# Performance work log

Measured on AMD Instinct MI355X. Metric: run time of the kernel, lower is better.

The kernel has to match this reference:

```python
import jax, jax.numpy as jnp
import numpy as np

GAMMA = 1.0        # softmin temperature
BANDWIDTH = 0      # 0 => no Sakoe-Chiba band (numba code only skips when 0 < bw < |i-j|)
BIG = 1e30         # finite stand-in for +inf: exp(-BIG/gamma) underflows to exactly 0 in fp32,
                   # reproducing the inf-initialized R/SigR softmin ratios without NaNs
B, N, M = 32, 512, 512


def setup_inputs() -> dict:
    k1, k2 = jax.random.split(jax.random.key(0))
    D = jax.random.uniform(k1, (B, N, M), dtype=jnp.float32)    # pairwise distances (>= 0)
    Sig = jax.random.uniform(k2, (B, N, M), dtype=jnp.float32)  # per-cell uncertainty
    return {"D": D, "Sig": Sig}


def _soft_dtw(D, Sig):
    """uDTW forward DP (compute_softdtw), vectorized over anti-diagonal wavefronts.
    Returns jnp.stack([R[:, N, M], SigR[:, N, M]]) of shape (2, B)."""
    b, n, m = D.shape
    alpha = 1.0 / GAMMA
    # Dp[i, j] == D_new[i, j] = D[i-1, j-1] with zero border (indices 0..N, 0..M)
    Dp = jnp.pad(D, ((0, 0), (1, 0), (1, 0)))
    Sp = jnp.pad(Sig, ((0, 0), (1, 0), (1, 0)))
    iarr = jnp.arange(n + 1)

    def diag(A, d):
        # A[:, i, d - i] for i = 0..N, zero where j out of [0, M]
        j = d - iarr
        vals = A[:, iarr, jnp.clip(j, 0, m)]
        return jnp.where((j >= 0) & (j <= m), vals, 0.0)

    def shift(x, fill):
        # x[:, i-1] (index i-1 along the diagonal buffer)
        return jnp.concatenate([jnp.full((b, 1), fill, x.dtype), x[:, :-1]], axis=1)

    # diagonal buffers indexed by i; diag d=0 holds R[0,0]=0, rest inf(BIG); diag d=1 all inf
    r2 = jnp.full((b, n + 1), BIG, jnp.float32).at[:, 0].set(0.0)
    r1 = jnp.full((b, n + 1), BIG, jnp.float32)
    s2 = jnp.full((b, n + 1), BIG, jnp.float32).at[:, 0].set(0.0)
    s1 = jnp.full((b, n + 1), BIG, jnp.float32)

    def step(carry, d):
        r2, r1, s2, s1 = carry  # R/SigR diagonals d-2 and d-1
        j = d - iarr
        valid = (iarr >= 1) & (j >= 1) & (j <= m)
        if BANDWIDTH > 0:
            valid = valid & (jnp.abs(iarr - j) <= BANDWIDTH)
        # softmin ratios from R neighbors: (i-1,j-1)=prev2 shifted, (i-1,j)=prev1 shifted, (i,j-1)=prev1
        rr0 = -alpha * shift(r2, BIG)
        rr1 = -alpha * shift(r1, BIG)
        rr2 = -alpha * r1
        rmax = jnp.maximum(jnp.maximum(rr0, rr1), rr2)
        e0 = jnp.exp(rr0 - rmax)
        e1 = jnp.exp(rr1 - rmax)
        e2 = jnp.exp(rr2 - rmax)
        inv = 1.0 / (e0 + e1 + e2)
        p0, p1, p2 = e0 * inv, e1 * inv, e2 * inv
        dDd, dD1, dD2 = diag(Dp, d), diag(Dp, d - 1), diag(Dp, d - 2)
        dSd, dS1, dS2 = diag(Sp, d), diag(Sp, d - 1), diag(Sp, d - 2)
        # R[i,j] = D[i-1,j-1] + softmin-weighted avg of D_new neighbors (uDTW recurrence)
        newR = jnp.where(valid, dDd + p0 * shift(dD2, 0.0) + p1 * shift(dD1, 0.0) + p2 * dD1, BIG)
        newS = jnp.where(valid, dSd + p0 * shift(dS2, 0.0) + p1 * shift(dS1, 0.0) + p2 * dS1, BIG)
        return (r1, newR, s1, newS), None

    (_, rlast, _, slast), _ = jax.lax.scan(step, (r2, r1, s2, s1), jnp.arange(2, n + m + 1))
    # last anti-diagonal d = N + M contains cell (N, M) at index i = N
    return jnp.stack([rlast[:, n], slast[:, n]])  # (2, B)


def reference(D, Sig):
    return _soft_dtw(D, Sig)
```

## Files before the change

### kernel.cpp

```cpp
#include <hip/hip_runtime.h>


constexpr int N = 512;
constexpr int M = 512;
constexpr int BATCH = 32;
constexpr int NM = N + M;
constexpr int K = 32;
constexpr int NB = 32;
constexpr int PHASES = NB + 7;
constexpr float NL2E = -1.4426950408889634f;
constexpr float NLN2 = -0.6931471805599453f;
constexpr float EPS  = 1e-30f;

__device__ __forceinline__ float lane_shr1_or(float oldv, float x) {
  return __int_as_float(__builtin_amdgcn_update_dpp(
      __float_as_int(oldv), __float_as_int(x), 0x138, 0xf, 0xf, false));
}
__device__ __forceinline__ int qclamp(int q) {
  return q < 0 ? 0 : (q > 127 ? 127 : q);
}

__global__ __launch_bounds__(512, 2)
void softdtw_fwd(const float* __restrict__ D,
                 const float* __restrict__ Sig,
                 float* __restrict__ out) {
  const int b = blockIdx.x;
  const int t = threadIdx.x;
  const int w = t >> 6;
  const float4* Drow4 = (const float4*)(D + ((size_t)b * N + t) * M);

  __shared__ float2 edge[8][640];
  __shared__ __align__(16) float zpad[64];
  for (int idx = t; idx < 8 * 640; idx += 512)
    ((float2*)edge)[idx] = make_float2(0.f, 0.f);
  if (t < 64) zpad[t] = 0.f;

  float eSelf = 0.f, dSelfL = 0.f;
  float eN2 = (t == 0) ? 1.f : 0.f, dN2L = 0.f;

  const int Bl = 2 * w, Bh = 2 * w + 17;

  float4 r0, r1, r2, r3, r4, r5, r6, r7, r8;
  {
    const int q = (32 * Bl - t) >> 2;
    r0 = Drow4[qclamp(q + 0)]; r1 = Drow4[qclamp(q + 1)];
    r2 = Drow4[qclamp(q + 2)]; r3 = Drow4[qclamp(q + 3)];
    r4 = Drow4[qclamp(q + 4)]; r5 = Drow4[qclamp(q + 5)];
    r6 = Drow4[qclamp(q + 6)]; r7 = Drow4[qclamp(q + 7)];
    r8 = Drow4[qclamp(q + 8)];
  }
  __syncthreads();

  for (int p = 0; p < PHASES; ++p) {
    const int B = p - w;
    const int nB = B + 1;
    const bool dopre = (nB >= Bl) && (nB <= Bh);

    if (B >= Bl && B <= Bh) {
      const int d0 = 2 + B * K;
      const int c0 = d0 - t - 2;

      const float4* ep = (w > 0)
          ? (const float4*)&edge[w - 1][64 + (d0 - 64 * w - 2)]
          : (const float4*)zpad;

      const float4 n0 = ep[0], n1 = ep[1], n2 = ep[2], n3 = ep[3];

      const int s = c0 & 3;
      const bool s2 = (s & 2) != 0, s1b = (s & 1) != 0;
      const float
        f0 = r0.x, f1 = r0.y, f2 = r0.z, f3 = r0.w,
        f4 = r1.x, f5 = r1.y, f6 = r1.z, f7 = r1.w,
        f8 = r2.x, f9 = r2.y, f10 = r2.z, f11 = r2.w,
        f12 = r3.x, f13 = r3.y, f14 = r3.z, f15 = r3.w,
        f16 = r4.x, f17 = r4.y, f18 = r4.z, f19 = r4.w,
        f20 = r5.x, f21 = r5.y, f22 = r5.z, f23 = r5.w,
        f24 = r6.x, f25 = r6.y, f26 = r6.z, f27 = r6.w,
        f28 = r7.x, f29 = r7.y, f30 = r7.z, f31 = r7.w,
        f32 = r8.x, f33 = r8.y, f34 = r8.z, f35 = r8.w;
      const float
        x0  = s2 ? f2  : f0,  x1  = s2 ? f3  : f1,  x2  = s2 ? f4  : f2,
        x3  = s2 ? f5  : f3,  x4  = s2 ? f6  : f4,  x5  = s2 ? f7  : f5,
        x6  = s2 ? f8  : f6,  x7  = s2 ? f9  : f7,  x8  = s2 ? f10 : f8,
        x9  = s2 ? f11 : f9,  x10 = s2 ? f12 : f10, x11 = s2 ? f13 : f11,
        x12 = s2 ? f14 : f12, x13 = s2 ? f15 : f13, x14 = s2 ? f16 : f14,
        x15 = s2 ? f17 : f15, x16 = s2 ? f18 : f16, x17 = s2 ? f19 : f17,
        x18 = s2 ? f20 : f18, x19 = s2 ? f21 : f19, x20 = s2 ? f22 : f20,
        x21 = s2 ? f23 : f21, x22 = s2 ? f24 : f22, x23 = s2 ? f25 : f23,
        x24 = s2 ? f26 : f24, x25 = s2 ? f27 : f25, x26 = s2 ? f28 : f26,
        x27 = s2 ? f29 : f27, x28 = s2 ? f30 : f28, x29 = s2 ? f31 : f29,
        x30 = s2 ? f32 : f30, x31 = s2 ? f33 : f31, x32 = s2 ? f34 : f32;
      const float
        g0  = s1b ? x1  : x0,  g1  = s1b ? x2  : x1,  g2  = s1b ? x3  : x2,
        g3  = s1b ? x4  : x3,  g4  = s1b ? x5  : x4,  g5  = s1b ? x6  : x5,
        g6  = s1b ? x7  : x6,  g7  = s1b ? x8  : x7,  g8  = s1b ? x9  : x8,
        g9  = s1b ? x10 : x9,  g10 = s1b ? x11 : x10, g11 = s1b ? x12 : x11,
        g12 = s1b ? x13 : x12, g13 = s1b ? x14 : x13, g14 = s1b ? x15 : x14,
        g15 = s1b ? x16 : x15, g16 = s1b ? x17 : x16, g17 = s1b ? x18 : x17,
        g18 = s1b ? x19 : x18, g19 = s1b ? x20 : x19, g20 = s1b ? x21 : x20,
        g21 = s1b ? x22 : x21, g22 = s1b ? x23 : x22, g23 = s1b ? x24 : x23,
        g24 = s1b ? x25 : x24, g25 = s1b ? x26 : x25, g26 = s1b ? x27 : x26,
        g27 = s1b ? x28 : x27, g28 = s1b ? x29 : x28, g29 = s1b ? x30 : x29,
        g30 = s1b ? x31 : x30, g31 = s1b ? x32 : x31;

      if (dopre) {
        const int q = (32 * nB - t) >> 2;
        r0 = Drow4[qclamp(q + 0)]; r1 = Drow4[qclamp(q + 1)];
        r2 = Drow4[qclamp(q + 2)]; r3 = Drow4[qclamp(q + 3)];
        r4 = Drow4[qclamp(q + 4)]; r5 = Drow4[qclamp(q + 5)];
        r6 = Drow4[qclamp(q + 6)]; r7 = Drow4[qclamp(q + 7)];
        r8 = Drow4[qclamp(q + 8)];
      }

      const float4 n4 = ep[4], n5 = ep[5], n6 = ep[6], n7 = ep[7];

      float2* eput = &edge[w][64 + c0];

#define STEP(kk, NE, ND)                                                       \
      {                                                                        \
        const int c = c0 + (kk);                                               \
        const bool valid = ((unsigned)c) < 512u;                               \
        const float ddL = (g##kk) * NL2E;                                      \
        const float ddLm = valid ? ddL : -1e30f;                               \
        const float sE = lane_shr1_or((NE), eSelf);                            \
        const float sD = lane_shr1_or((ND), dSelfL);                           \
        const float e0 = eN2, e2 = eSelf;                                      \
        const float s02 = (e0 + e2) + EPS;                                     \
        const float sum = s02 + sE;                                            \
        const float inv = __builtin_amdgcn_rcpf(sum);                          \
        const float numL = fmaf(e0, dN2L, fmaf(sE, sD, e2 * dSelfL));          \
        const float rr = fmaf(inv, numL, ddLm);                                \
        const float newE = __builtin_amdgcn_exp2f(rr);                         \
        if (d0 + (kk) == NM && t == N - 1) {                                   \
          const float* Sb = Sig + (size_t)b * N * M;                           \
          const float sgA = Sb[(size_t)(N - 1) * M + (M - 1)];                 \
          const float sg0 = Sb[(size_t)(N - 2) * M + (M - 2)];                 \
          const float sg1 = Sb[(size_t)(N - 2) * M + (M - 1)];                 \
          const float sg2 = Sb[(size_t)(N - 1) * M + (M - 2)];                 \
          out[b] = rr * NLN2;                                                  \
          out[BATCH + b] = sgA + inv * (e0 * sg0 + sE * sg1 + e2 * sg2);       \
        }                                                                      \
        eN2 = sE; dN2L = sD;                                                   \
        eSelf = newE; dSelfL = ddL;                                            \
        eput[kk] = make_float2(newE, ddL);                                     \
      }
#define STEP2(m, NQ)                                                           \
      STEP(2 * m,     NQ.x, NQ.y)                                              \
      STEP(2 * m + 1, NQ.z, NQ.w)

      STEP(0,  n0.x, n0.y)  STEP(1,  n0.z, n0.w)
      STEP(2,  n1.x, n1.y)  STEP(3,  n1.z, n1.w)
      STEP(4,  n2.x, n2.y)  STEP(5,  n2.z, n2.w)
      STEP(6,  n3.x, n3.y)  STEP(7,  n3.z, n3.w)

      const float4 n8 = ep[8], n9 = ep[9], n10 = ep[10], n11 = ep[11];

      STEP(8,  n4.x, n4.y)  STEP(9,  n4.z, n4.w)
      STEP(10, n5.x, n5.y)  STEP(11, n5.z, n5.w)
      STEP(12, n6.x, n6.y)  STEP(13, n6.z, n6.w)
      STEP(14, n7.x, n7.y)  STEP(15, n7.z, n7.w)

      const float4 n12 = ep[12], n13 = ep[13], n14 = ep[14], n15 = ep[15];

      STEP(16, n8.x,  n8.y)   STEP(17, n8.z,  n8.w)
      STEP(18, n9.x,  n9.y)   STEP(19, n9.z,  n9.w)
      STEP(20, n10.x, n10.y)  STEP(21, n10.z, n10.w)
      STEP(22, n11.x, n11.y)  STEP(23, n11.z, n11.w)

      STEP(24, n12.x, n12.y)  STEP(25, n12.z, n12.w)
      STEP(26, n13.x, n13.y)  STEP(27, n13.z, n13.w)
      STEP(28, n14.x, n14.y)  STEP(29, n14.z, n14.w)
      STEP(30, n15.x, n15.y)  STEP(31, n15.z, n15.w)
#undef STEP2
#undef STEP
    } else if (dopre) {
      const int q = (32 * nB - t) >> 2;
      r0 = Drow4[qclamp(q + 0)]; r1 = Drow4[qclamp(q + 1)];
      r2 = Drow4[qclamp(q + 2)]; r3 = Drow4[qclamp(q + 3)];
      r4 = Drow4[qclamp(q + 4)]; r5 = Drow4[qclamp(q + 5)];
      r6 = Drow4[qclamp(q + 6)]; r7 = Drow4[qclamp(q + 7)];
      r8 = Drow4[qclamp(q + 8)];
    }

    __syncthreads();
  }
}

extern "C" void kernel_launch(void* const* d_in, const int* in_sizes, int n_in,
                              void* d_out, int out_size, void* d_ws, size_t ws_size,
                              hipStream_t stream) {
  const float* D   = (const float*)d_in[0];
  const float* Sig = (const float*)d_in[1];
  float* out = (float*)d_out;
  softdtw_fwd<<<dim3(BATCH), dim3(512), 0, stream>>>(D, Sig, out);
}
```

Before: 177.8 us.

## Double wavefront block width to halve phase count and barriers

Raises the diagonal block size from 32 to 64, so each wave processes 64 anti-diagonal steps per phase and the number of block-synchronised phases drops from 39 to 23. It prefetches the next D block in two chunks interleaved with the compute, and replaces __syncthreads with an explicit LDS wait plus a raw s_barrier. The aim is to cut barrier and pipeline fill/drain overhead. In exchange, register pressure roughly doubles for the D window (17 float4s plus 64 selected values) at 512 threads with 2 blocks per SM, which risks spills, and the raw barrier skips the vmcnt wait.

```diff
diff --git a/kernel.cpp b/kernel.cpp
--- a/kernel.cpp
+++ b/kernel.cpp
@@ -5,9 +5,9 @@
 constexpr int M = 512;
 constexpr int BATCH = 32;
 constexpr int NM = N + M;
-constexpr int K = 32;
-constexpr int NB = 32;
-constexpr int PHASES = NB + 7;
+constexpr int K = 64;
+constexpr int NB = 16;
+constexpr int PHASES = 23;
 constexpr float NL2E = -1.4426950408889634f;
 constexpr float NLN2 = -0.6931471805599453f;
 constexpr float EPS  = 1e-30f;
@@ -30,89 +30,64 @@
   const float4* Drow4 = (const float4*)(D + ((size_t)b * N + t) * M);
 
   __shared__ float2 edge[8][640];
-  __shared__ __align__(16) float zpad[64];
+  __shared__ __align__(16) float zpad[128];
   for (int idx = t; idx < 8 * 640; idx += 512)
     ((float2*)edge)[idx] = make_float2(0.f, 0.f);
-  if (t < 64) zpad[t] = 0.f;
+  if (t < 128) zpad[t] = 0.f;
 
   float eSelf = 0.f, dSelfL = 0.f;
   float eN2 = (t == 0) ? 1.f : 0.f, dN2L = 0.f;
 
-  const int Bl = 2 * w, Bh = 2 * w + 17;
-
-  float4 r0, r1, r2, r3, r4, r5, r6, r7, r8;
+  const int Bl = w, Bh = w + 8;
+
+  float4 r0,r1,r2,r3,r4,r5,r6,r7,r8,r9,r10,r11,r12,r13,r14,r15,r16;
   {
-    const int q = (32 * Bl - t) >> 2;
-    r0 = Drow4[qclamp(q + 0)]; r1 = Drow4[qclamp(q + 1)];
-    r2 = Drow4[qclamp(q + 2)]; r3 = Drow4[qclamp(q + 3)];
-    r4 = Drow4[qclamp(q + 4)]; r5 = Drow4[qclamp(q + 5)];
-    r6 = Drow4[qclamp(q + 6)]; r7 = Drow4[qclamp(q + 7)];
-    r8 = Drow4[qclamp(q + 8)];
+    const int q = (K * Bl - t) >> 2;
+    r0 = Drow4[qclamp(q + 0)];  r1 = Drow4[qclamp(q + 1)];
+    r2 = Drow4[qclamp(q + 2)];  r3 = Drow4[qclamp(q + 3)];
+    r4 = Drow4[qclamp(q + 4)];  r5 = Drow4[qclamp(q + 5)];
+    r6 = Drow4[qclamp(q + 6)];  r7 = Drow4[qclamp(q + 7)];
+    r8 = Drow4[qclamp(q + 8)];  r9 = Drow4[qclamp(q + 9)];
+    r10 = Drow4[qclamp(q + 10)]; r11 = Drow4[qclamp(q + 11)];
+    r12 = Drow4[qclamp(q + 12)]; r13 = Drow4[qclamp(q + 13)];
+    r14 = Drow4[qclamp(q + 14)]; r15 = Drow4[qclamp(q + 15)];
+    r16 = Drow4[qclamp(q + 16)];
   }
   __syncthreads();
 
   for (int p = 0; p < PHASES; ++p) {
     const int B = p - w;
-    const int nB = B + 1;
-    const bool dopre = (nB >= Bl) && (nB <= Bh);
+    const int Bn = B + 1;
+    const bool dopre = (Bn >= Bl) && (Bn <= Bh);
 
     if (B >= Bl && B <= Bh) {
       const int d0 = 2 + B * K;
-      const int c0 = d0 - t - 2;
+      const int c0 = K * B - t;
 
       const float4* ep = (w > 0)
-          ? (const float4*)&edge[w - 1][64 + (d0 - 64 * w - 2)]
+          ? (const float4*)&edge[w - 1][64 + K * (B - w)]
           : (const float4*)zpad;
 
-      const float4 n0 = ep[0], n1 = ep[1], n2 = ep[2], n3 = ep[3];
+      const float4 na0 = ep[0], na1 = ep[1], na2 = ep[2], na3 = ep[3];
 
       const int s = c0 & 3;
       const bool s2 = (s & 2) != 0, s1b = (s & 1) != 0;
-      const float
-        f0 = r0.x, f1 = r0.y, f2 = r0.z, f3 = r0.w,
-        f4 = r1.x, f5 = r1.y, f6 = r1.z, f7 = r1.w,
-        f8 = r2.x, f9 = r2.y, f10 = r2.z, f11 = r2.w,
-        f12 = r3.x, f13 = r3.y, f14 = r3.z, f15 = r3.w,
-        f16 = r4.x, f17 = r4.y, f18 = r4.z, f19 = r4.w,
-        f20 = r5.x, f21 = r5.y, f22 = r5.z, f23 = r5.w,
-        f24 = r6.x, f25 = r6.y, f26 = r6.z, f27 = r6.w,
-        f28 = r7.x, f29 = r7.y, f30 = r7.z, f31 = r7.w,
-        f32 = r8.x, f33 = r8.y, f34 = r8.z, f35 = r8.w;
-      const float
-        x0  = s2 ? f2  : f0,  x1  = s2 ? f3  : f1,  x2  = s2 ? f4  : f2,
-        x3  = s2 ? f5  : f3,  x4  = s2 ? f6  : f4,  x5  = s2 ? f7  : f5,
-        x6  = s2 ? f8  : f6,  x7  = s2 ? f9  : f7,  x8  = s2 ? f10 : f8,
-        x9  = s2 ? f11 : f9,  x10 = s2 ? f12 : f10, x11 = s2 ? f13 : f11,
-        x12 = s2 ? f14 : f12, x13 = s2 ? f15 : f13, x14 = s2 ? f16 : f14,
-        x15 = s2 ? f17 : f15, x16 = s2 ? f18 : f16, x17 = s2 ? f19 : f17,
-        x18 = s2 ? f20 : f18, x19 = s2 ? f21 : f19, x20 = s2 ? f22 : f20,
-        x21 = s2 ? f23 : f21, x22 = s2 ? f24 : f22, x23 = s2 ? f25 : f23,
-        x24 = s2 ? f26 : f24, x25 = s2 ? f27 : f25, x26 = s2 ? f28 : f26,
-        x27 = s2 ? f29 : f27, x28 = s2 ? f30 : f28, x29 = s2 ? f31 : f29,
-        x30 = s2 ? f32 : f30, x31 = s2 ? f33 : f31, x32 = s2 ? f34 : f32;
-      const float
-        g0  = s1b ? x1  : x0,  g1  = s1b ? x2  : x1,  g2  = s1b ? x3  : x2,
-        g3  = s1b ? x4  : x3,  g4  = s1b ? x5  : x4,  g5  = s1b ? x6  : x5,
-        g6  = s1b ? x7  : x6,  g7  = s1b ? x8  : x7,  g8  = s1b ? x9  : x8,
-        g9  = s1b ? x10 : x9,  g10 = s1b ? x11 : x10, g11 = s1b ? x12 : x11,
-        g12 = s1b ? x13 : x12, g13 = s1b ? x14 : x13, g14 = s1b ? x15 : x14,
-        g15 = s1b ? x16 : x15, g16 = s1b ? x17 : x16, g17 = s1b ? x18 : x17,
-        g18 = s1b ? x19 : x18, g19 = s1b ? x20 : x19, g20 = s1b ? x21 : x20,
-        g21 = s1b ? x22 : x21, g22 = s1b ? x23 : x22, g23 = s1b ? x24 : x23,
-        g24 = s1b ? x25 : x24, g25 = s1b ? x26 : x25, g26 = s1b ? x27 : x26,
-        g27 = s1b ? x28 : x27, g28 = s1b ? x29 : x28, g29 = s1b ? x30 : x29,
-        g30 = s1b ? x31 : x30, g31 = s1b ? x32 : x31;
-
-      if (dopre) {
-        const int q = (32 * nB - t) >> 2;
-        r0 = Drow4[qclamp(q + 0)]; r1 = Drow4[qclamp(q + 1)];
-        r2 = Drow4[qclamp(q + 2)]; r3 = Drow4[qclamp(q + 3)];
-        r4 = Drow4[qclamp(q + 4)]; r5 = Drow4[qclamp(q + 5)];
-        r6 = Drow4[qclamp(q + 6)]; r7 = Drow4[qclamp(q + 7)];
-        r8 = Drow4[qclamp(q + 8)];
-      }
-
-      const float4 n4 = ep[4], n5 = ep[5], n6 = ep[6], n7 = ep[7];
+      float f[68];
+#define UNP(i, R) f[4*(i)] = (R).x; f[4*(i)+1] = (R).y; \
+                  f[4*(i)+2] = (R).z; f[4*(i)+3] = (R).w;
+      UNP(0, r0)  UNP(1, r1)  UNP(2, r2)  UNP(3, r3)  UNP(4, r4)
+      UNP(5, r5)  UNP(6, r6)  UNP(7, r7)  UNP(8, r8)  UNP(9, r9)
+      UNP(10, r10) UNP(11, r11) UNP(12, r12) UNP(13, r13)
+      UNP(14, r14) UNP(15, r15) UNP(16, r16)
+#undef UNP
+      float g[64];
+      {
+        float x[65];
+#pragma unroll
+        for (int e = 0; e < 65; ++e) x[e] = s2 ? f[e + 2] : f[e];
+#pragma unroll
+        for (int e = 0; e < 64; ++e) g[e] = s1b ? x[e + 1] : x[e];
+      }
 
       float2* eput = &edge[w][64 + c0];
 
@@ -120,7 +95,7 @@
       {                                                                        \
         const int c = c0 + (kk);                                               \
         const bool valid = ((unsigned)c) < 512u;                               \
-        const float ddL = (g##kk) * NL2E;                                      \
+        const float ddL = g[kk] * NL2E;                                        \
         const float ddLm = valid ? ddL : -1e30f;                               \
         const float sE = lane_shr1_or((NE), eSelf);                            \
         const float sD = lane_shr1_or((ND), dSelfL);                           \
@@ -144,45 +119,93 @@
         eSelf = newE; dSelfL = ddL;                                            \
         eput[kk] = make_float2(newE, ddL);                                     \
       }
-#define STEP2(m, NQ)                                                           \
-      STEP(2 * m,     NQ.x, NQ.y)                                              \
-      STEP(2 * m + 1, NQ.z, NQ.w)
-
-      STEP(0,  n0.x, n0.y)  STEP(1,  n0.z, n0.w)
-      STEP(2,  n1.x, n1.y)  STEP(3,  n1.z, n1.w)
-      STEP(4,  n2.x, n2.y)  STEP(5,  n2.z, n2.w)
-      STEP(6,  n3.x, n3.y)  STEP(7,  n3.z, n3.w)
-
-      const float4 n8 = ep[8], n9 = ep[9], n10 = ep[10], n11 = ep[11];
-
-      STEP(8,  n4.x, n4.y)  STEP(9,  n4.z, n4.w)
-      STEP(10, n5.x, n5.y)  STEP(11, n5.z, n5.w)
-      STEP(12, n6.x, n6.y)  STEP(13, n6.z, n6.w)
-      STEP(14, n7.x, n7.y)  STEP(15, n7.z, n7.w)
-
-      const float4 n12 = ep[12], n13 = ep[13], n14 = ep[14], n15 = ep[15];
-
-      STEP(16, n8.x,  n8.y)   STEP(17, n8.z,  n8.w)
-      STEP(18, n9.x,  n9.y)   STEP(19, n9.z,  n9.w)
-      STEP(20, n10.x, n10.y)  STEP(21, n10.z, n10.w)
-      STEP(22, n11.x, n11.y)  STEP(23, n11.z, n11.w)
-
-      STEP(24, n12.x, n12.y)  STEP(25, n12.z, n12.w)
-      STEP(26, n13.x, n13.y)  STEP(27, n13.z, n13.w)
-      STEP(28, n14.x, n14.y)  STEP(29, n14.z, n14.w)
-      STEP(30, n15.x, n15.y)  STEP(31, n15.z, n15.w)
-#undef STEP2
+
+      const float4 nb0 = ep[4], nb1 = ep[5], nb2 = ep[6], nb3 = ep[7];
+
+      STEP(0,  na0.x, na0.y)  STEP(1,  na0.z, na0.w)
+      STEP(2,  na1.x, na1.y)  STEP(3,  na1.z, na1.w)
+      STEP(4,  na2.x, na2.y)  STEP(5,  na2.z, na2.w)
+      STEP(6,  na3.x, na3.y)  STEP(7,  na3.z, na3.w)
+
+      const float4 nc0 = ep[8], nc1 = ep[9], nc2 = ep[10], nc3 = ep[11];
+
+      STEP(8,  nb0.x, nb0.y)  STEP(9,  nb0.z, nb0.w)
+      STEP(10, nb1.x, nb1.y)  STEP(11, nb1.z, nb1.w)
+      STEP(12, nb2.x, nb2.y)  STEP(13, nb2.z, nb2.w)
+      STEP(14, nb3.x, nb3.y)  STEP(15, nb3.z, nb3.w)
+
+      const float4 nd0 = ep[12], nd1 = ep[13], nd2 = ep[14], nd3 = ep[15];
+
+      STEP(16, nc0.x, nc0.y)  STEP(17, nc0.z, nc0.w)
+      STEP(18, nc1.x, nc1.y)  STEP(19, nc1.z, nc1.w)
+      STEP(20, nc2.x, nc2.y)  STEP(21, nc2.z, nc2.w)
+      STEP(22, nc3.x, nc3.y)  STEP(23, nc3.z, nc3.w)
+
+      const float4 ne0 = ep[16], ne1 = ep[17], ne2 = ep[18], ne3 = ep[19];
+
+      STEP(24, nd0.x, nd0.y)  STEP(25, nd0.z, nd0.w)
+      STEP(26, nd1.x, nd1.y)  STEP(27, nd1.z, nd1.w)
+      STEP(28, nd2.x, nd2.y)  STEP(29, nd2.z, nd2.w)
+      STEP(30, nd3.x, nd3.y)  STEP(31, nd3.z, nd3.w)
+
+      if (dopre) {
+        const int q = (K * Bn - t) >> 2;
+        r0 = Drow4[qclamp(q + 0)];  r1 = Drow4[qclamp(q + 1)];
+        r2 = Drow4[qclamp(q + 2)];  r3 = Drow4[qclamp(q + 3)];
+        r4 = Drow4[qclamp(q + 4)];  r5 = Drow4[qclamp(q + 5)];
+        r6 = Drow4[qclamp(q + 6)];  r7 = Drow4[qclamp(q + 7)];
+        r8 = Drow4[qclamp(q + 8)];
+      }
+
+      const float4 nf0 = ep[20], nf1 = ep[21], nf2 = ep[22], nf3 = ep[23];
+
+      STEP(32, ne0.x, ne0.y)  STEP(33, ne0.z, ne0.w)
+      STEP(34, ne1.x, ne1.y)  STEP(35, ne1.z, ne1.w)
+      STEP(36, ne2.x, ne2.y)  STEP(37, ne2.z, ne2.w)
+      STEP(38, ne3.x, ne3.y)  STEP(39, ne3.z, ne3.w)
+
+      const float4 ng0 = ep[24], ng1 = ep[25], ng2 = ep[26], ng3 = ep[27];
+
+      STEP(40, nf0.x, nf0.y)  STEP(41, nf0.z, nf0.w)
+      STEP(42, nf1.x, nf1.y)  STEP(43, nf1.z, nf1.w)
+      STEP(44, nf2.x, nf2.y)  STEP(45, nf2.z, nf2.w)
+      STEP(46, nf3.x, nf3.y)  STEP(47, nf3.z, nf3.w)
+
+      const float4 nh0 = ep[28], nh1 = ep[29], nh2 = ep[30], nh3 = ep[31];
+
+      STEP(48, ng0.x, ng0.y)  STEP(49, ng0.z, ng0.w)
+      STEP(50, ng1.x, ng1.y)  STEP(51, ng1.z, ng1.w)
+      STEP(52, ng2.x, ng2.y)  STEP(53, ng2.z, ng2.w)
+      STEP(54, ng3.x, ng3.y)  STEP(55, ng3.z, ng3.w)
+
+      if (dopre) {
+        const int q = (K * Bn - t) >> 2;
+        r9 = Drow4[qclamp(q + 9)];   r10 = Drow4[qclamp(q + 10)];
+        r11 = Drow4[qclamp(q + 11)]; r12 = Drow4[qclamp(q + 12)];
+        r13 = Drow4[qclamp(q + 13)]; r14 = Drow4[qclamp(q + 14)];
+        r15 = Drow4[qclamp(q + 15)]; r16 = Drow4[qclamp(q + 16)];
+      }
+
+      STEP(56, nh0.x, nh0.y)  STEP(57, nh0.z, nh0.w)
+      STEP(58, nh1.x, nh1.y)  STEP(59, nh1.z, nh1.w)
+      STEP(60, nh2.x, nh2.y)  STEP(61, nh2.z, nh2.w)
+      STEP(62, nh3.x, nh3.y)  STEP(63, nh3.z, nh3.w)
 #undef STEP
     } else if (dopre) {
-      const int q = (32 * nB - t) >> 2;
-      r0 = Drow4[qclamp(q + 0)]; r1 = Drow4[qclamp(q + 1)];
-      r2 = Drow4[qclamp(q + 2)]; r3 = Drow4[qclamp(q + 3)];
-      r4 = Drow4[qclamp(q + 4)]; r5 = Drow4[qclamp(q + 5)];
-      r6 = Drow4[qclamp(q + 6)]; r7 = Drow4[qclamp(q + 7)];
-      r8 = Drow4[qclamp(q + 8)];
+      const int q = (K * Bn - t) >> 2;
+      r0 = Drow4[qclamp(q + 0)];  r1 = Drow4[qclamp(q + 1)];
+      r2 = Drow4[qclamp(q + 2)];  r3 = Drow4[qclamp(q + 3)];
+      r4 = Drow4[qclamp(q + 4)];  r5 = Drow4[qclamp(q + 5)];
+      r6 = Drow4[qclamp(q + 6)];  r7 = Drow4[qclamp(q + 7)];
+      r8 = Drow4[qclamp(q + 8)];  r9 = Drow4[qclamp(q + 9)];
+      r10 = Drow4[qclamp(q + 10)]; r11 = Drow4[qclamp(q + 11)];
+      r12 = Drow4[qclamp(q + 12)]; r13 = Drow4[qclamp(q + 13)];
+      r14 = Drow4[qclamp(q + 14)]; r15 = Drow4[qclamp(q + 15)];
+      r16 = Drow4[qclamp(q + 16)];
     }
 
-    __syncthreads();
+    asm volatile("s_waitcnt lgkmcnt(0)" ::: "memory");
+    __builtin_amdgcn_s_barrier();
   }
 }
 
```

New measurement: 336.0 us. 89.0% more time.
